# Kernel tuning notes

Hardware: AMD Instinct MI355X
Metric: run time of the kernel (lower is better)

The kernel has to match this reference:

```python
import jax, jax.numpy as jnp
import numpy as np

HEADS = 16
DIM_HEAD = 64
LN_EPS = 1e-3  # keras LayerNormalization default


def setup_inputs() -> dict:
    key = jax.random.key(0)
    ks = jax.random.split(key, 4)
    B, N, D = 8, 512, 1024
    inner = HEADS * DIM_HEAD  # 1024
    return {
        "x": jax.random.normal(ks[0], (B, N, D), dtype=jnp.float32),
        "w_qkv": jax.random.normal(ks[1], (D, 3 * inner), dtype=jnp.float32) * (D ** -0.5),
        "reattn_w": jax.random.normal(ks[2], (HEADS, HEADS), dtype=jnp.float32),
        "ln_gamma": jnp.ones((HEADS,), dtype=jnp.float32),
        "ln_beta": jnp.zeros((HEADS,), dtype=jnp.float32),
        "w_out": jax.random.normal(ks[3], (inner, D), dtype=jnp.float32) * (inner ** -0.5),
        "b_out": jnp.zeros((D,), dtype=jnp.float32),
    }


def reference(x, w_qkv, reattn_w, ln_gamma, ln_beta, w_out, b_out):
    B, N, D = x.shape
    H, dh = HEADS, DIM_HEAD
    scale = dh ** -0.5

    qkv = x @ w_qkv  # [B, N, 3*H*dh]
    q, k, v = jnp.split(qkv, 3, axis=-1)
    # b n (h d) -> b h n d
    to_heads = lambda t: t.reshape(B, N, H, dh).transpose(0, 2, 1, 3)
    q, k, v = to_heads(q), to_heads(k), to_heads(v)

    dots = jnp.einsum("bhid,bhjd->bhij", q, k) * scale  # [B, H, N, N]
    attn = jax.nn.softmax(dots, axis=-1)

    # re-attention: mix across heads
    attn = jnp.einsum("bhij,hg->bgij", attn, reattn_w)

    # LayerNorm over the head axis (axis=1), keras default eps
    mean = jnp.mean(attn, axis=1, keepdims=True)
    var = jnp.var(attn, axis=1, keepdims=True)
    attn = (attn - mean) * jax.lax.rsqrt(var + LN_EPS)
    attn = attn * ln_gamma[None, :, None, None] + ln_beta[None, :, None, None]

    out = jnp.einsum("bhij,bhjd->bhid", attn, v)  # [B, H, N, dh]
    out = out.transpose(0, 2, 1, 3).reshape(B, N, H * dh)  # b h n d -> b n (h d)
    return out @ w_out + b_out
```

## Files before the change

### kernel.cpp

```cpp
#include <hip/hip_runtime.h>
#include <math.h>

#define BB 8
#define NN 512
#define DD 1024
#define HH 16
#define DH 64
#define INNER 1024
#define QKV3 3072

typedef __attribute__((ext_vector_type(8))) short short8;
typedef __attribute__((ext_vector_type(4))) float f32x4;

__device__ __forceinline__ float4 ld4(const float* p) { return *(const float4*)p; }

__device__ __forceinline__ unsigned short f2bf(float f) {
    unsigned u = __float_as_uint(f);
    return (unsigned short)((u + 0x7fffu + ((u >> 16) & 1u)) >> 16);
}
__device__ __forceinline__ float bf2f(unsigned short u) {
    return __uint_as_float(((unsigned)u) << 16);
}

__global__ void conv_bf16(const float* __restrict__ in, unsigned short* __restrict__ out) {
    size_t i = ((size_t)blockIdx.x * 256 + threadIdx.x) * 4;
    float4 v = ld4(in + i);
    ushort4 o;
    o.x = f2bf(v.x); o.y = f2bf(v.y); o.z = f2bf(v.z); o.w = f2bf(v.w);
    *(ushort4*)(out + i) = o;
}

__global__ void convT_bf16(const float* __restrict__ in, unsigned short* __restrict__ out,
                           int K, int N) {
    __shared__ float t[32][33];
    const int n0 = blockIdx.x * 32, k0 = blockIdx.y * 32;
    const int tx = threadIdx.x & 31, ty = threadIdx.x >> 5;
#pragma unroll
    for (int l = 0; l < 4; ++l)
        t[ty + 8 * l][tx] = in[(size_t)(k0 + ty + 8 * l) * N + n0 + tx];
    __syncthreads();
#pragma unroll
    for (int l = 0; l < 4; ++l)
        out[(size_t)(n0 + ty + 8 * l) * K + k0 + tx] = f2bf(t[tx][ty + 8 * l]);
}

__global__ __launch_bounds__(256) void gemm_bf16(
    const unsigned short* __restrict__ A, const unsigned short* __restrict__ Bt,
    float* __restrict__ C, const float* __restrict__ bias, int M, int N, int K) {
    __shared__ short As[128 * 32];
    __shared__ short Bs[128 * 32];
    const int tid = threadIdx.x;
    const int w = tid >> 6, l = tid & 63;
    const int bm = blockIdx.y * 128, bn = blockIdx.x * 128;
    const int wm = (w >> 1) * 64, wn = (w & 1) * 64;
    const int lrow = l & 15, lq = l >> 4;

    f32x4 acc[4][4];
#pragma unroll
    for (int i = 0; i < 4; ++i)
#pragma unroll
        for (int j = 0; j < 4; ++j) acc[i][j] = (f32x4){0.f, 0.f, 0.f, 0.f};

    for (int k0 = 0; k0 < K; k0 += 32) {
#pragma unroll
        for (int t = 0; t < 2; ++t) {
            const int q = w * 2 + t;
            const int li = q * 512 + l * 8;
            const int row = li >> 5, kc = li & 31;
            const unsigned short* ga = A + (size_t)(bm + row) * K + k0 + kc;
            __builtin_amdgcn_global_load_lds(
                (const __attribute__((address_space(1))) void*)ga,
                (__attribute__((address_space(3))) void*)(As + q * 512), 16, 0, 0);
            const unsigned short* gb = Bt + (size_t)(bn + row) * K + k0 + kc;
            __builtin_amdgcn_global_load_lds(
                (const __attribute__((address_space(1))) void*)gb,
                (__attribute__((address_space(3))) void*)(Bs + q * 512), 16, 0, 0);
        }
        __syncthreads();

        short8 a[4], b[4];
#pragma unroll
        for (int i = 0; i < 4; ++i)
            a[i] = *(const short8*)(As + (wm + i * 16 + lrow) * 32 + lq * 8);
#pragma unroll
        for (int j = 0; j < 4; ++j)
            b[j] = *(const short8*)(Bs + (wn + j * 16 + lrow) * 32 + lq * 8);
#pragma unroll
        for (int i = 0; i < 4; ++i)
#pragma unroll
            for (int j = 0; j < 4; ++j)
                acc[i][j] = __builtin_amdgcn_mfma_f32_16x16x32_bf16(a[i], b[j], acc[i][j], 0, 0, 0);
        __syncthreads();
    }

#pragma unroll
    for (int i = 0; i < 4; ++i)
#pragma unroll
        for (int j = 0; j < 4; ++j) {
            const int col = bn + wn + j * 16 + lrow;
            const float bv = bias ? bias[col] : 0.f;
#pragma unroll
            for (int r = 0; r < 4; ++r) {
                const int row = bm + wm + i * 16 + lq * 4 + r;
                C[(size_t)row * N + col] = acc[i][j][r] + bv;
            }
        }
}

__global__ __launch_bounds__(256) void gemm_bf16_bf(
    const unsigned short* __restrict__ A, const unsigned short* __restrict__ Bt,
    unsigned short* __restrict__ C, int M, int N, int K) {
    __shared__ short As[128 * 32];
    __shared__ short Bs[128 * 32];
    const int tid = threadIdx.x;
    const int w = tid >> 6, l = tid & 63;
    const int bm = blockIdx.y * 128, bn = blockIdx.x * 128;
    const int wm = (w >> 1) * 64, wn = (w & 1) * 64;
    const int lrow = l & 15, lq = l >> 4;

    f32x4 acc[4][4];
#pragma unroll
    for (int i = 0; i < 4; ++i)
#pragma unroll
        for (int j = 0; j < 4; ++j) acc[i][j] = (f32x4){0.f, 0.f, 0.f, 0.f};

    for (int k0 = 0; k0 < K; k0 += 32) {
#pragma unroll
        for (int t = 0; t < 2; ++t) {
            const int q = w * 2 + t;
            const int li = q * 512 + l * 8;
            const int row = li >> 5, kc = li & 31;
            const unsigned short* ga = A + (size_t)(bm + row) * K + k0 + kc;
            __builtin_amdgcn_global_load_lds(
                (const __attribute__((address_space(1))) void*)ga,
                (__attribute__((address_space(3))) void*)(As + q * 512), 16, 0, 0);
            const unsigned short* gb = Bt + (size_t)(bn + row) * K + k0 + kc;
            __builtin_amdgcn_global_load_lds(
                (const __attribute__((address_space(1))) void*)gb,
                (__attribute__((address_space(3))) void*)(Bs + q * 512), 16, 0, 0);
        }
        __syncthreads();

        short8 a[4], b[4];
#pragma unroll
        for (int i = 0; i < 4; ++i)
            a[i] = *(const short8*)(As + (wm + i * 16 + lrow) * 32 + lq * 8);
#pragma unroll
        for (int j = 0; j < 4; ++j)
            b[j] = *(const short8*)(Bs + (wn + j * 16 + lrow) * 32 + lq * 8);
#pragma unroll
        for (int i = 0; i < 4; ++i)
#pragma unroll
            for (int j = 0; j < 4; ++j)
                acc[i][j] = __builtin_amdgcn_mfma_f32_16x16x32_bf16(a[i], b[j], acc[i][j], 0, 0, 0);
        __syncthreads();
    }

#pragma unroll
    for (int i = 0; i < 4; ++i)
#pragma unroll
        for (int j = 0; j < 4; ++j) {
            const int col = bn + wn + j * 16 + lrow;
#pragma unroll
            for (int r = 0; r < 4; ++r) {
                const int row = bm + wm + i * 16 + lq * 4 + r;
                C[(size_t)row * N + col] = f2bf(acc[i][j][r]);
            }
        }
}

__global__ __launch_bounds__(256) void scores_stream(
    const unsigned short* __restrict__ qkvb, unsigned short* __restrict__ attnb,
    float* __restrict__ lsum) {
    const int bh = blockIdx.y;
    const int h = bh & 15, b = bh >> 4;
    const int w = threadIdx.x >> 6, l = threadIdx.x & 63;
    const int i0 = blockIdx.x * 64 + w * 16;
    const int lrow = l & 15, lq = l >> 4;

    const unsigned short* qb = qkvb + (size_t)(b * NN) * QKV3 + h * DH + lq * 8;
    const unsigned short* kb = qkvb + (size_t)(b * NN) * QKV3 + INNER + h * DH + lq * 8;

    const short8 qf0 = *(const short8*)(qb + (size_t)(i0 + lrow) * QKV3);
    const short8 qf1 = *(const short8*)(qb + (size_t)(i0 + lrow) * QKV3 + 32);

    const unsigned short* krow = kb + (size_t)lrow * QKV3;
    unsigned short* orow = attnb + ((size_t)bh * NN + i0 + lrow) * NN + lq * 4;

    float lacc = 0.f;
#pragma unroll 4
    for (int jt = 0; jt < 32; ++jt) {
        const unsigned short* kp = krow + (size_t)jt * 16 * QKV3;
        short8 kf0 = *(const short8*)(kp);
        short8 kf1 = *(const short8*)(kp + 32);
        f32x4 acc = (f32x4){0.f, 0.f, 0.f, 0.f};
        acc = __builtin_amdgcn_mfma_f32_16x16x32_bf16(kf0, qf0, acc, 0, 0, 0);
        acc = __builtin_amdgcn_mfma_f32_16x16x32_bf16(kf1, qf1, acc, 0, 0, 0);
        float e0 = __expf(acc[0] * 0.125f);
        float e1 = __expf(acc[1] * 0.125f);
        float e2 = __expf(acc[2] * 0.125f);
        float e3 = __expf(acc[3] * 0.125f);
        lacc += (e0 + e1) + (e2 + e3);
        ushort4 o;
        o.x = f2bf(e0); o.y = f2bf(e1); o.z = f2bf(e2); o.w = f2bf(e3);
        *(ushort4*)(orow + jt * 16) = o;
    }
    lacc += __shfl_xor(lacc, 16, 64);
    lacc += __shfl_xor(lacc, 32, 64);
    if (lq == 0) lsum[(size_t)bh * NN + i0 + lrow] = lacc;
}

__global__ void reattn_ln_bf(unsigned short* __restrict__ attnb,
                             const float* __restrict__ lsum,
                             const float* __restrict__ rw,
                             const float* __restrict__ gamma,
                             const float* __restrict__ beta) {
    __shared__ float w[16][16];
    __shared__ float gs[16], bs[16];
    const int tid = threadIdx.x;
    ((float*)w)[tid] = rw[tid];
    if (tid < 16) { gs[tid] = gamma[tid]; bs[tid] = beta[tid]; }
    __syncthreads();

    const size_t idx = (size_t)blockIdx.x * 256 + tid;
    const int j4 = (int)(idx & 127);
    const int i = (int)((idx >> 7) & 511);
    const int b = (int)(idx >> 16);
    const size_t hstr = (size_t)NN * NN;
    unsigned short* base = attnb + (size_t)b * HH * hstr + (size_t)i * NN + j4 * 4;
    const float* lrow = lsum + (size_t)(b * HH) * NN + i;

    float v[16][4];
#pragma unroll
    for (int h = 0; h < 16; ++h) {
        const float linv = 1.0f / lrow[h * NN];
        ushort4 u = *(const ushort4*)(base + h * hstr);
        v[h][0] = bf2f(u.x) * linv; v[h][1] = bf2f(u.y) * linv;
        v[h][2] = bf2f(u.z) * linv; v[h][3] = bf2f(u.w) * linv;
    }
    float o[16][4];
    float me[4] = {0.f, 0.f, 0.f, 0.f};
#pragma unroll
    for (int g = 0; g < 16; ++g) {
        float s0 = 0.f, s1 = 0.f, s2 = 0.f, s3 = 0.f;
#pragma unroll
        for (int h = 0; h < 16; ++h) {
            const float wg = w[h][g];
            s0 += v[h][0] * wg; s1 += v[h][1] * wg;
            s2 += v[h][2] * wg; s3 += v[h][3] * wg;
        }
        o[g][0] = s0; o[g][1] = s1; o[g][2] = s2; o[g][3] = s3;
        me[0] += s0; me[1] += s1; me[2] += s2; me[3] += s3;
    }
#pragma unroll
    for (int r = 0; r < 4; ++r) me[r] *= 0.0625f;
    float va[4] = {0.f, 0.f, 0.f, 0.f};
#pragma unroll
    for (int g = 0; g < 16; ++g)
#pragma unroll
        for (int r = 0; r < 4; ++r) {
            float d = o[g][r] - me[r];
            va[r] += d * d;
        }
    float ri[4];
#pragma unroll
    for (int r = 0; r < 4; ++r) ri[r] = rsqrtf(va[r] * 0.0625f + 1e-3f);
#pragma unroll
    for (int g = 0; g < 16; ++g) {
        ushort4 u;
        u.x = f2bf((o[g][0] - me[0]) * ri[0] * gs[g] + bs[g]);
        u.y = f2bf((o[g][1] - me[1]) * ri[1] * gs[g] + bs[g]);
        u.z = f2bf((o[g][2] - me[2]) * ri[2] * gs[g] + bs[g]);
        u.w = f2bf((o[g][3] - me[3]) * ri[3] * gs[g] + bs[g]);
        *(ushort4*)(base + g * hstr) = u;
    }
}

__global__ void transpose_v(const unsigned short* __restrict__ qkvb,
                            unsigned short* __restrict__ vT) {
    __shared__ unsigned short t[32][33];
    const int bh = blockIdx.z;
    const int h = bh & 15, b = bh >> 4;
    const int j0 = blockIdx.x * 32, d0 = blockIdx.y * 32;
    const int tx = threadIdx.x & 31, ty = threadIdx.x >> 5;
    const unsigned short* src = qkvb + (size_t)(b * NN) * QKV3 + 2 * INNER + h * DH;
#pragma unroll
    for (int k = 0; k < 4; ++k)
        t[ty + 8 * k][tx] = src[(size_t)(j0 + ty + 8 * k) * QKV3 + d0 + tx];
    __syncthreads();
    unsigned short* dst = vT + (size_t)bh * DH * NN;
#pragma unroll
    for (int k = 0; k < 4; ++k)
        dst[(size_t)(d0 + ty + 8 * k) * NN + j0 + tx] = t[tx][ty + 8 * k];
}

__global__ __launch_bounds__(256) void pv_mfma(
    const unsigned short* __restrict__ attnb, const unsigned short* __restrict__ vT,
    unsigned short* __restrict__ outhb) {
    const int bh = blockIdx.y;
    const int h = bh & 15, b = bh >> 4;
    const int i0 = blockIdx.x * 128;
    __shared__ short Ps[128 * 64];
    __shared__ short Vs[64 * 64];
    const int tid = threadIdx.x;
    const int w = tid >> 6, l = tid & 63;
    const int lrow = l & 15, lq = l >> 4;
    const int lr8 = l >> 3;
    const int swd = ((l & 7) ^ (lr8 & 7)) * 8;

    f32x4 acc[2][4];
#pragma unroll
    for (int ic = 0; ic < 2; ++ic)
#pragma unroll
        for (int dt = 0; dt < 4; ++dt) acc[ic][dt] = (f32x4){0.f, 0.f, 0.f, 0.f};

    const unsigned short* pb = attnb + ((size_t)bh * NN + i0) * NN;
    const unsigned short* vb = vT + (size_t)bh * DH * NN;

    for (int j0 = 0; j0 < NN; j0 += 64) {
#pragma unroll
        for (int t = 0; t < 4; ++t) {
            int c = w * 4 + t;
            int r = c * 8 + lr8;
            __builtin_amdgcn_global_load_lds(
                (const __attribute__((address_space(1))) void*)(pb + (size_t)r * NN + j0 + swd),
                (__attribute__((address_space(3))) void*)(Ps + c * 512), 16, 0, 0);
        }
#pragma unroll
        for (int t = 0; t < 2; ++t) {
            int c = w * 2 + t;
            int d = c * 8 + lr8;
            __builtin_amdgcn_global_load_lds(
                (const __attribute__((address_space(1))) void*)(vb + (size_t)d * NN + j0 + swd),
                (__attribute__((address_space(3))) void*)(Vs + c * 512), 16, 0, 0);
        }
        __syncthreads();

#pragma unroll
        for (int kh = 0; kh < 2; ++kh) {
            short8 vf[4];
#pragma unroll
            for (int dt = 0; dt < 4; ++dt)
                vf[dt] = *(const short8*)(Vs + (dt * 16 + lrow) * 64 + (((kh * 4 + lq) ^ (lrow & 7)) * 8));
#pragma unroll
            for (int ic = 0; ic < 2; ++ic) {
                short8 pf = *(const short8*)(Ps + (w * 32 + ic * 16 + lrow) * 64 + (((kh * 4 + lq) ^ (lrow & 7)) * 8));
#pragma unroll
                for (int dt = 0; dt < 4; ++dt)
                    acc[ic][dt] = __builtin_amdgcn_mfma_f32_16x16x32_bf16(vf[dt], pf, acc[ic][dt], 0, 0, 0);
            }
        }
        __syncthreads();
    }

#pragma unroll
    for (int ic = 0; ic < 2; ++ic) {
        unsigned short* orow = outhb +
            ((size_t)(b * NN + i0 + w * 32 + ic * 16 + lrow)) * INNER + h * DH + lq * 4;
#pragma unroll
        for (int dt = 0; dt < 4; ++dt) {
            ushort4 o;
            o.x = f2bf(acc[ic][dt][0]); o.y = f2bf(acc[ic][dt][1]);
            o.z = f2bf(acc[ic][dt][2]); o.w = f2bf(acc[ic][dt][3]);
            *(ushort4*)(orow + dt * 16) = o;
        }
    }
}

extern "C" void kernel_launch(void* const* d_in, const int* in_sizes, int n_in,
                              void* d_out, int out_size, void* d_ws, size_t ws_size,
                              hipStream_t stream) {
    const float* x        = (const float*)d_in[0];
    const float* w_qkv    = (const float*)d_in[1];
    const float* reattn_w = (const float*)d_in[2];
    const float* ln_gamma = (const float*)d_in[3];
    const float* ln_beta  = (const float*)d_in[4];
    const float* w_out    = (const float*)d_in[5];
    const float* b_out    = (const float*)d_in[6];
    float* out = (float*)d_out;

    unsigned short* qkvb  = (unsigned short*)d_ws;
    unsigned short* attnb = qkvb + (size_t)BB * NN * QKV3;
    unsigned short* vTb   = attnb + (size_t)BB * HH * NN * NN;
    unsigned short* outhb = vTb + (size_t)BB * HH * DH * NN;
    unsigned short* xb    = outhb + (size_t)BB * NN * INNER;
    unsigned short* wqkvT = xb + (size_t)BB * NN * DD;
    unsigned short* woutT = wqkvT + (size_t)DD * QKV3;
    float*          lsum  = (float*)(woutT + (size_t)INNER * INNER);

    dim3 blk(256);

    conv_bf16<<<dim3((BB * NN * DD) / 1024), blk, 0, stream>>>(x, xb);
    convT_bf16<<<dim3(QKV3 / 32, DD / 32), blk, 0, stream>>>(w_qkv, wqkvT, DD, QKV3);
    convT_bf16<<<dim3(INNER / 32, INNER / 32), blk, 0, stream>>>(w_out, woutT, INNER, INNER);

    gemm_bf16_bf<<<dim3(QKV3 / 128, (BB * NN) / 128), blk, 0, stream>>>(
        xb, wqkvT, qkvb, BB * NN, QKV3, DD);

    scores_stream<<<dim3(NN / 64, BB * HH), blk, 0, stream>>>(qkvb, attnb, lsum);

    reattn_ln_bf<<<dim3((BB * NN * NN) / 1024), blk, 0, stream>>>(
        attnb, lsum, reattn_w, ln_gamma, ln_beta);

    transpose_v<<<dim3(NN / 32, DH / 32, BB * HH), blk, 0, stream>>>(qkvb, vTb);

    pv_mfma<<<dim3(NN / 128, BB * HH), blk, 0, stream>>>(attnb, vTb, outhb);

    gemm_bf16<<<dim3(INNER / 128, (BB * NN) / 128), blk, 0, stream>>>(
        outhb, woutT, out, b_out, BB * NN, INNER, INNER);
}
```

Before: 246.4 us.

## Split scores kernel over key halves and software-pipeline K loads

```diff
diff --git a/kernel.cpp b/kernel.cpp
--- a/kernel.cpp
+++ b/kernel.cpp
@@ -171,9 +171,10 @@
 
 __global__ __launch_bounds__(256) void scores_stream(
     const unsigned short* __restrict__ qkvb, unsigned short* __restrict__ attnb,
-    float* __restrict__ lsum) {
-    const int bh = blockIdx.y;
+    float* __restrict__ lsum2) {
+    const int bh = blockIdx.z;
     const int h = bh & 15, b = bh >> 4;
+    const int jh = blockIdx.y;
     const int w = threadIdx.x >> 6, l = threadIdx.x & 63;
     const int i0 = blockIdx.x * 64 + w * 16;
     const int lrow = l & 15, lq = l >> 4;
@@ -184,15 +185,27 @@
     const short8 qf0 = *(const short8*)(qb + (size_t)(i0 + lrow) * QKV3);
     const short8 qf1 = *(const short8*)(qb + (size_t)(i0 + lrow) * QKV3 + 32);
 
-    const unsigned short* krow = kb + (size_t)lrow * QKV3;
-    unsigned short* orow = attnb + ((size_t)bh * NN + i0 + lrow) * NN + lq * 4;
+    const unsigned short* krow = kb + (size_t)(jh * 256 + lrow) * QKV3;
+    unsigned short* orow = attnb + ((size_t)bh * NN + i0 + lrow) * NN + jh * 256 + lq * 4;
+
+    short8 ka[4], kc[4];
+#pragma unroll
+    for (int p = 0; p < 4; ++p) {
+        const unsigned short* kp = krow + (size_t)p * 16 * QKV3;
+        ka[p] = *(const short8*)(kp);
+        kc[p] = *(const short8*)(kp + 32);
+    }
 
     float lacc = 0.f;
-#pragma unroll 4
-    for (int jt = 0; jt < 32; ++jt) {
-        const unsigned short* kp = krow + (size_t)jt * 16 * QKV3;
-        short8 kf0 = *(const short8*)(kp);
-        short8 kf1 = *(const short8*)(kp + 32);
+#pragma unroll
+    for (int jt = 0; jt < 16; ++jt) {
+        const int s = jt & 3;
+        short8 kf0 = ka[s], kf1 = kc[s];
+        if (jt < 12) {
+            const unsigned short* kp = krow + (size_t)(jt + 4) * 16 * QKV3;
+            ka[s] = *(const short8*)(kp);
+            kc[s] = *(const short8*)(kp + 32);
+        }
         f32x4 acc = (f32x4){0.f, 0.f, 0.f, 0.f};
         acc = __builtin_amdgcn_mfma_f32_16x16x32_bf16(kf0, qf0, acc, 0, 0, 0);
         acc = __builtin_amdgcn_mfma_f32_16x16x32_bf16(kf1, qf1, acc, 0, 0, 0);
@@ -207,11 +220,12 @@
     }
     lacc += __shfl_xor(lacc, 16, 64);
     lacc += __shfl_xor(lacc, 32, 64);
-    if (lq == 0) lsum[(size_t)bh * NN + i0 + lrow] = lacc;
+    if (lq == 0)
+        lsum2[(size_t)jh * BB * HH * NN + (size_t)bh * NN + i0 + lrow] = lacc;
 }
 
 __global__ void reattn_ln_bf(unsigned short* __restrict__ attnb,
-                             const float* __restrict__ lsum,
+                             const float* __restrict__ lsum2,
                              const float* __restrict__ rw,
                              const float* __restrict__ gamma,
                              const float* __restrict__ beta) {
@@ -228,12 +242,13 @@
     const int b = (int)(idx >> 16);
     const size_t hstr = (size_t)NN * NN;
     unsigned short* base = attnb + (size_t)b * HH * hstr + (size_t)i * NN + j4 * 4;
-    const float* lrow = lsum + (size_t)(b * HH) * NN + i;
+    const float* l0 = lsum2 + (size_t)(b * HH) * NN + i;
+    const float* l1 = l0 + (size_t)BB * HH * NN;
 
     float v[16][4];
 #pragma unroll
     for (int h = 0; h < 16; ++h) {
-        const float linv = 1.0f / lrow[h * NN];
+        const float linv = 1.0f / (l0[h * NN] + l1[h * NN]);
         ushort4 u = *(const ushort4*)(base + h * hstr);
         v[h][0] = bf2f(u.x) * linv; v[h][1] = bf2f(u.y) * linv;
         v[h][2] = bf2f(u.z) * linv; v[h][3] = bf2f(u.w) * linv;
@@ -386,7 +401,7 @@
     unsigned short* xb    = outhb + (size_t)BB * NN * INNER;
     unsigned short* wqkvT = xb + (size_t)BB * NN * DD;
     unsigned short* woutT = wqkvT + (size_t)DD * QKV3;
-    float*          lsum  = (float*)(woutT + (size_t)INNER * INNER);
+    float*          lsum2 = (float*)(woutT + (size_t)INNER * INNER);
 
     dim3 blk(256);
 
@@ -397,10 +412,10 @@
     gemm_bf16_bf<<<dim3(QKV3 / 128, (BB * NN) / 128), blk, 0, stream>>>(
         xb, wqkvT, qkvb, BB * NN, QKV3, DD);
 
-    scores_stream<<<dim3(NN / 64, BB * HH), blk, 0, stream>>>(qkvb, attnb, lsum);
+    scores_stream<<<dim3(NN / 64, 2, BB * HH), blk, 0, stream>>>(qkvb, attnb, lsum2);
 
     reattn_ln_bf<<<dim3((BB * NN * NN) / 1024), blk, 0, stream>>>(
-        attnb, lsum, reattn_w, ln_gamma, ln_beta);
+        attnb, lsum2, reattn_w, ln_gamma, ln_beta);
 
     transpose_v<<<dim3(NN / 32, DH / 32, BB * HH), blk, 0, stream>>>(qkvb, vTb);
 
```

After: 247.4 us. No clear change (+0.4%).

## Fuse scores, re-attention LayerNorm and PV into one attention kernel

Applied to the files above, without the earlier changes.

```diff
diff --git a/kernel.cpp b/kernel.cpp
--- a/kernel.cpp
+++ b/kernel.cpp
@@ -8,6 +8,9 @@
 #define DH 64
 #define INNER 1024
 #define QKV3 3072
+
+#define RS 152
+#define PS 2440
 
 typedef __attribute__((ext_vector_type(8))) short short8;
 typedef __attribute__((ext_vector_type(4))) float f32x4;
@@ -169,23 +172,48 @@
         }
 }
 
-__global__ __launch_bounds__(256) void scores_stream(
-    const unsigned short* __restrict__ qkvb, unsigned short* __restrict__ attnb,
-    float* __restrict__ lsum) {
-    const int bh = blockIdx.y;
+__global__ void transpose_v(const unsigned short* __restrict__ qkvb,
+                            unsigned short* __restrict__ vT) {
+    __shared__ unsigned short t[32][33];
+    const int bh = blockIdx.z;
     const int h = bh & 15, b = bh >> 4;
-    const int w = threadIdx.x >> 6, l = threadIdx.x & 63;
-    const int i0 = blockIdx.x * 64 + w * 16;
+    const int j0 = blockIdx.x * 32, d0 = blockIdx.y * 32;
+    const int tx = threadIdx.x & 31, ty = threadIdx.x >> 5;
+    const unsigned short* src = qkvb + (size_t)(b * NN) * QKV3 + 2 * INNER + h * DH;
+#pragma unroll
+    for (int k = 0; k < 4; ++k)
+        t[ty + 8 * k][tx] = src[(size_t)(j0 + ty + 8 * k) * QKV3 + d0 + tx];
+    __syncthreads();
+    unsigned short* dst = vT + (size_t)bh * DH * NN;
+#pragma unroll
+    for (int k = 0; k < 4; ++k)
+        dst[(size_t)(d0 + ty + 8 * k) * NN + j0 + tx] = t[tx][ty + 8 * k];
+}
+
+__global__ __launch_bounds__(1024) void attn_fused(
+    const unsigned short* __restrict__ qkvb, const unsigned short* __restrict__ vT,
+    unsigned short* __restrict__ outhb, const float* __restrict__ rw,
+    const float* __restrict__ gamma, const float* __restrict__ beta) {
+    __shared__ unsigned short P[16 * PS];
+    __shared__ float wmix[16][16];
+    __shared__ float gs[16], bs[16];
+
+    const int b = blockIdx.y;
+    const int i0 = blockIdx.x * 16;
+    const int tid = threadIdx.x;
+    const int h = tid >> 6;
+    const int l = tid & 63;
     const int lrow = l & 15, lq = l >> 4;
 
-    const unsigned short* qb = qkvb + (size_t)(b * NN) * QKV3 + h * DH + lq * 8;
-    const unsigned short* kb = qkvb + (size_t)(b * NN) * QKV3 + INNER + h * DH + lq * 8;
-
-    const short8 qf0 = *(const short8*)(qb + (size_t)(i0 + lrow) * QKV3);
-    const short8 qf1 = *(const short8*)(qb + (size_t)(i0 + lrow) * QKV3 + 32);
-
-    const unsigned short* krow = kb + (size_t)lrow * QKV3;
-    unsigned short* orow = attnb + ((size_t)bh * NN + i0 + lrow) * NN + lq * 4;
+    if (tid < 256) ((float*)wmix)[tid] = rw[tid];
+    if (tid < 16) { gs[tid] = gamma[tid]; bs[tid] = beta[tid]; }
+
+    const unsigned short* qp = qkvb + (size_t)(b * NN + i0 + lrow) * QKV3 + h * DH + lq * 8;
+    const short8 qf0 = *(const short8*)(qp);
+    const short8 qf1 = *(const short8*)(qp + 32);
+
+    const unsigned short* krow =
+        qkvb + (size_t)(b * NN + lrow) * QKV3 + INNER + h * DH + lq * 8;
 
     float lacc = 0.f;
 #pragma unroll 4
@@ -196,174 +224,89 @@
         f32x4 acc = (f32x4){0.f, 0.f, 0.f, 0.f};
         acc = __builtin_amdgcn_mfma_f32_16x16x32_bf16(kf0, qf0, acc, 0, 0, 0);
         acc = __builtin_amdgcn_mfma_f32_16x16x32_bf16(kf1, qf1, acc, 0, 0, 0);
-        float e0 = __expf(acc[0] * 0.125f);
-        float e1 = __expf(acc[1] * 0.125f);
-        float e2 = __expf(acc[2] * 0.125f);
-        float e3 = __expf(acc[3] * 0.125f);
-        lacc += (e0 + e1) + (e2 + e3);
-        ushort4 o;
-        o.x = f2bf(e0); o.y = f2bf(e1); o.z = f2bf(e2); o.w = f2bf(e3);
-        *(ushort4*)(orow + jt * 16) = o;
+        lacc += (__expf(acc[0] * 0.125f) + __expf(acc[1] * 0.125f)) +
+                (__expf(acc[2] * 0.125f) + __expf(acc[3] * 0.125f));
     }
     lacc += __shfl_xor(lacc, 16, 64);
     lacc += __shfl_xor(lacc, 32, 64);
-    if (lq == 0) lsum[(size_t)bh * NN + i0 + lrow] = lacc;
-}
-
-__global__ void reattn_ln_bf(unsigned short* __restrict__ attnb,
-                             const float* __restrict__ lsum,
-                             const float* __restrict__ rw,
-                             const float* __restrict__ gamma,
-                             const float* __restrict__ beta) {
-    __shared__ float w[16][16];
-    __shared__ float gs[16], bs[16];
-    const int tid = threadIdx.x;
-    ((float*)w)[tid] = rw[tid];
-    if (tid < 16) { gs[tid] = gamma[tid]; bs[tid] = beta[tid]; }
-    __syncthreads();
-
-    const size_t idx = (size_t)blockIdx.x * 256 + tid;
-    const int j4 = (int)(idx & 127);
-    const int i = (int)((idx >> 7) & 511);
-    const int b = (int)(idx >> 16);
-    const size_t hstr = (size_t)NN * NN;
-    unsigned short* base = attnb + (size_t)b * HH * hstr + (size_t)i * NN + j4 * 4;
-    const float* lrow = lsum + (size_t)(b * HH) * NN + i;
-
-    float v[16][4];
-#pragma unroll
-    for (int h = 0; h < 16; ++h) {
-        const float linv = 1.0f / lrow[h * NN];
-        ushort4 u = *(const ushort4*)(base + h * hstr);
-        v[h][0] = bf2f(u.x) * linv; v[h][1] = bf2f(u.y) * linv;
-        v[h][2] = bf2f(u.z) * linv; v[h][3] = bf2f(u.w) * linv;
-    }
-    float o[16][4];
-    float me[4] = {0.f, 0.f, 0.f, 0.f};
-#pragma unroll
-    for (int g = 0; g < 16; ++g) {
-        float s0 = 0.f, s1 = 0.f, s2 = 0.f, s3 = 0.f;
-#pragma unroll
-        for (int h = 0; h < 16; ++h) {
-            const float wg = w[h][g];
-            s0 += v[h][0] * wg; s1 += v[h][1] * wg;
-            s2 += v[h][2] * wg; s3 += v[h][3] * wg;
-        }
-        o[g][0] = s0; o[g][1] = s1; o[g][2] = s2; o[g][3] = s3;
-        me[0] += s0; me[1] += s1; me[2] += s2; me[3] += s3;
-    }
-#pragma unroll
-    for (int r = 0; r < 4; ++r) me[r] *= 0.0625f;
-    float va[4] = {0.f, 0.f, 0.f, 0.f};
-#pragma unroll
-    for (int g = 0; g < 16; ++g)
-#pragma unroll
-        for (int r = 0; r < 4; ++r) {
-            float d = o[g][r] - me[r];
-            va[r] += d * d;
-        }
-    float ri[4];
-#pragma unroll
-    for (int r = 0; r < 4; ++r) ri[r] = rsqrtf(va[r] * 0.0625f + 1e-3f);
-#pragma unroll
-    for (int g = 0; g < 16; ++g) {
-        ushort4 u;
-        u.x = f2bf((o[g][0] - me[0]) * ri[0] * gs[g] + bs[g]);
-        u.y = f2bf((o[g][1] - me[1]) * ri[1] * gs[g] + bs[g]);
-        u.z = f2bf((o[g][2] - me[2]) * ri[2] * gs[g] + bs[g]);
-        u.w = f2bf((o[g][3] - me[3]) * ri[3] * gs[g] + bs[g]);
-        *(ushort4*)(base + g * hstr) = u;
-    }
-}
-
-__global__ void transpose_v(const unsigned short* __restrict__ qkvb,
-                            unsigned short* __restrict__ vT) {
-    __shared__ unsigned short t[32][33];
-    const int bh = blockIdx.z;
-    const int h = bh & 15, b = bh >> 4;
-    const int j0 = blockIdx.x * 32, d0 = blockIdx.y * 32;
-    const int tx = threadIdx.x & 31, ty = threadIdx.x >> 5;
-    const unsigned short* src = qkvb + (size_t)(b * NN) * QKV3 + 2 * INNER + h * DH;
-#pragma unroll
-    for (int k = 0; k < 4; ++k)
-        t[ty + 8 * k][tx] = src[(size_t)(j0 + ty + 8 * k) * QKV3 + d0 + tx];
-    __syncthreads();
-    unsigned short* dst = vT + (size_t)bh * DH * NN;
-#pragma unroll
-    for (int k = 0; k < 4; ++k)
-        dst[(size_t)(d0 + ty + 8 * k) * NN + j0 + tx] = t[tx][ty + 8 * k];
-}
-
-__global__ __launch_bounds__(256) void pv_mfma(
-    const unsigned short* __restrict__ attnb, const unsigned short* __restrict__ vT,
-    unsigned short* __restrict__ outhb) {
-    const int bh = blockIdx.y;
-    const int h = bh & 15, b = bh >> 4;
-    const int i0 = blockIdx.x * 128;
-    __shared__ short Ps[128 * 64];
-    __shared__ short Vs[64 * 64];
-    const int tid = threadIdx.x;
-    const int w = tid >> 6, l = tid & 63;
-    const int lrow = l & 15, lq = l >> 4;
-    const int lr8 = l >> 3;
-    const int swd = ((l & 7) ^ (lr8 & 7)) * 8;
-
-    f32x4 acc[2][4];
-#pragma unroll
-    for (int ic = 0; ic < 2; ++ic)
-#pragma unroll
-        for (int dt = 0; dt < 4; ++dt) acc[ic][dt] = (f32x4){0.f, 0.f, 0.f, 0.f};
-
-    const unsigned short* pb = attnb + ((size_t)bh * NN + i0) * NN;
-    const unsigned short* vb = vT + (size_t)bh * DH * NN;
-
-    for (int j0 = 0; j0 < NN; j0 += 64) {
-#pragma unroll
-        for (int t = 0; t < 4; ++t) {
-            int c = w * 4 + t;
-            int r = c * 8 + lr8;
-            __builtin_amdgcn_global_load_lds(
-                (const __attribute__((address_space(1))) void*)(pb + (size_t)r * NN + j0 + swd),
-                (__attribute__((address_space(3))) void*)(Ps + c * 512), 16, 0, 0);
-        }
-#pragma unroll
-        for (int t = 0; t < 2; ++t) {
-            int c = w * 2 + t;
-            int d = c * 8 + lr8;
-            __builtin_amdgcn_global_load_lds(
-                (const __attribute__((address_space(1))) void*)(vb + (size_t)d * NN + j0 + swd),
-                (__attribute__((address_space(3))) void*)(Vs + c * 512), 16, 0, 0);
-        }
-        __syncthreads();
-
-#pragma unroll
-        for (int kh = 0; kh < 2; ++kh) {
-            short8 vf[4];
-#pragma unroll
-            for (int dt = 0; dt < 4; ++dt)
-                vf[dt] = *(const short8*)(Vs + (dt * 16 + lrow) * 64 + (((kh * 4 + lq) ^ (lrow & 7)) * 8));
-#pragma unroll
-            for (int ic = 0; ic < 2; ++ic) {
-                short8 pf = *(const short8*)(Ps + (w * 32 + ic * 16 + lrow) * 64 + (((kh * 4 + lq) ^ (lrow & 7)) * 8));
-#pragma unroll
-                for (int dt = 0; dt < 4; ++dt)
-                    acc[ic][dt] = __builtin_amdgcn_mfma_f32_16x16x32_bf16(vf[dt], pf, acc[ic][dt], 0, 0, 0);
-            }
-        }
-        __syncthreads();
-    }
-
-#pragma unroll
-    for (int ic = 0; ic < 2; ++ic) {
-        unsigned short* orow = outhb +
-            ((size_t)(b * NN + i0 + w * 32 + ic * 16 + lrow)) * INNER + h * DH + lq * 4;
-#pragma unroll
-        for (int dt = 0; dt < 4; ++dt) {
+    const float linv = 1.0f / lacc;
+
+    f32x4 oacc[4];
+#pragma unroll
+    for (int dt = 0; dt < 4; ++dt) oacc[dt] = (f32x4){0.f, 0.f, 0.f, 0.f};
+
+    const unsigned short* vb = vT + (size_t)(b * HH + h) * DH * NN;
+    const int mi = tid >> 6;
+    const int mj0 = (tid & 63) * 2;
+
+    for (int jc = 0; jc < 4; ++jc) {
+#pragma unroll
+        for (int s = 0; s < 8; ++s) {
+            const unsigned short* kp = krow + (size_t)(jc * 8 + s) * 16 * QKV3;
+            short8 kf0 = *(const short8*)(kp);
+            short8 kf1 = *(const short8*)(kp + 32);
+            f32x4 acc = (f32x4){0.f, 0.f, 0.f, 0.f};
+            acc = __builtin_amdgcn_mfma_f32_16x16x32_bf16(kf0, qf0, acc, 0, 0, 0);
+            acc = __builtin_amdgcn_mfma_f32_16x16x32_bf16(kf1, qf1, acc, 0, 0, 0);
             ushort4 o;
-            o.x = f2bf(acc[ic][dt][0]); o.y = f2bf(acc[ic][dt][1]);
-            o.z = f2bf(acc[ic][dt][2]); o.w = f2bf(acc[ic][dt][3]);
-            *(ushort4*)(orow + dt * 16) = o;
-        }
+            o.x = f2bf(__expf(acc[0] * 0.125f) * linv);
+            o.y = f2bf(__expf(acc[1] * 0.125f) * linv);
+            o.z = f2bf(__expf(acc[2] * 0.125f) * linv);
+            o.w = f2bf(__expf(acc[3] * 0.125f) * linv);
+            *(ushort4*)&P[h * PS + lrow * RS + s * 16 + lq * 4] = o;
+        }
+        __syncthreads();
+
+#pragma unroll
+        for (int jj = 0; jj < 2; ++jj) {
+            unsigned short* base = &P[mi * RS + mj0 + jj];
+            float v[16];
+#pragma unroll
+            for (int hh = 0; hh < 16; ++hh) v[hh] = bf2f(base[hh * PS]);
+            float o[16];
+            float me = 0.f;
+#pragma unroll
+            for (int g = 0; g < 16; ++g) {
+                float s = 0.f;
+#pragma unroll
+                for (int hh = 0; hh < 16; ++hh) s += v[hh] * wmix[hh][g];
+                o[g] = s;
+                me += s;
+            }
+            me *= 0.0625f;
+            float va = 0.f;
+#pragma unroll
+            for (int g = 0; g < 16; ++g) {
+                float d = o[g] - me;
+                va += d * d;
+            }
+            const float ri = rsqrtf(va * 0.0625f + 1e-3f);
+#pragma unroll
+            for (int g = 0; g < 16; ++g)
+                base[g * PS] = f2bf((o[g] - me) * ri * gs[g] + bs[g]);
+        }
+        __syncthreads();
+
+#pragma unroll
+        for (int jk = 0; jk < 4; ++jk) {
+            short8 pf = *(const short8*)&P[h * PS + lrow * RS + jk * 32 + lq * 8];
+#pragma unroll
+            for (int dt = 0; dt < 4; ++dt) {
+                short8 vf = *(const short8*)(vb + (size_t)(dt * 16 + lrow) * NN +
+                                             jc * 128 + jk * 32 + lq * 8);
+                oacc[dt] = __builtin_amdgcn_mfma_f32_16x16x32_bf16(vf, pf, oacc[dt], 0, 0, 0);
+            }
+        }
+        __syncthreads();
+    }
+
+    unsigned short* orow = outhb + (size_t)(b * NN + i0 + lrow) * INNER + h * DH + lq * 4;
+#pragma unroll
+    for (int dt = 0; dt < 4; ++dt) {
+        ushort4 o;
+        o.x = f2bf(oacc[dt][0]); o.y = f2bf(oacc[dt][1]);
+        o.z = f2bf(oacc[dt][2]); o.w = f2bf(oacc[dt][3]);
+        *(ushort4*)(orow + dt * 16) = o;
     }
 }
 
@@ -380,13 +323,11 @@
     float* out = (float*)d_out;
 
     unsigned short* qkvb  = (unsigned short*)d_ws;
-    unsigned short* attnb = qkvb + (size_t)BB * NN * QKV3;
-    unsigned short* vTb   = attnb + (size_t)BB * HH * NN * NN;
+    unsigned short* vTb   = qkvb + (size_t)BB * NN * QKV3;
     unsigned short* outhb = vTb + (size_t)BB * HH * DH * NN;
     unsigned short* xb    = outhb + (size_t)BB * NN * INNER;
     unsigned short* wqkvT = xb + (size_t)BB * NN * DD;
     unsigned short* woutT = wqkvT + (size_t)DD * QKV3;
-    float*          lsum  = (float*)(woutT + (size_t)INNER * INNER);
 
     dim3 blk(256);
 
@@ -397,14 +338,10 @@
     gemm_bf16_bf<<<dim3(QKV3 / 128, (BB * NN) / 128), blk, 0, stream>>>(
         xb, wqkvT, qkvb, BB * NN, QKV3, DD);
 
-    scores_stream<<<dim3(NN / 64, BB * HH), blk, 0, stream>>>(qkvb, attnb, lsum);
-
-    reattn_ln_bf<<<dim3((BB * NN * NN) / 1024), blk, 0, stream>>>(
-        attnb, lsum, reattn_w, ln_gamma, ln_beta);
-
     transpose_v<<<dim3(NN / 32, DH / 32, BB * HH), blk, 0, stream>>>(qkvb, vTb);
 
-    pv_mfma<<<dim3(NN / 128, BB * HH), blk, 0, stream>>>(attnb, vTb, outhb);
+    attn_fused<<<dim3(NN / 16, BB), dim3(1024), 0, stream>>>(
+        qkvb, vTb, outhb, reattn_w, ln_gamma, ln_beta);
 
     gemm_bf16<<<dim3(INNER / 128, (BB * NN) / 128), blk, 0, stream>>>(
         outhb, woutT, out, b_out, BB * NN, INNER, INNER);
```

New measurement: 288.8 us. 17.2% more time.
